# Kernel optimization log

Hardware: AMD Instinct MI355X
Metric: run time of the kernel (lower is better)

Reference implementation:

```python
import jax, jax.numpy as jnp
import numpy as np

B, T, C, L = 128, 512, 1024, 64
BLANK = C - 1          # keras ctc_batch_cost uses last class as blank
NEG = -1e9             # finite log-zero (grad-safe)
EPS = 1e-7             # keras.backend.epsilon()


def setup_inputs() -> dict:
    key = jax.random.key(0)
    k1, k2, k3, k4 = jax.random.split(key, 4)
    # y_pred: softmax probabilities, as ctc_batch_cost expects
    y_pred = jax.nn.softmax(jax.random.normal(k1, (B, T, C), dtype=jnp.float32), axis=-1)
    y_true = jax.random.randint(k2, (B, L), 0, BLANK).astype(jnp.int32)  # labels exclude blank
    input_length = jax.random.randint(k3, (B, 1), T // 2, T + 1).astype(jnp.int32)
    label_length = jax.random.randint(k4, (B, 1), L // 2, L + 1).astype(jnp.int32)
    return {"y_true": y_true, "y_pred": y_pred,
            "input_length": input_length, "label_length": label_length}


def _lse3(a, b, c):
    m = jnp.maximum(jnp.maximum(a, b), c)
    return m + jnp.log(jnp.exp(a - m) + jnp.exp(b - m) + jnp.exp(c - m))


def _ctc_loss(y_pred, y_true, input_length, label_length):
    # log probs, exactly as keras: log(y_pred + epsilon)
    logp = jnp.log(y_pred + EPS)                     # [B,T,C]
    Bsz, Tmax, _ = logp.shape
    Lm = y_true.shape[1]
    S = 2 * Lm + 1                                   # extended label length

    # extended labels: blank at even positions, labels at odd
    lab_ext = jnp.full((Bsz, S), BLANK, dtype=y_true.dtype).at[:, 1::2].set(y_true)
    s_idx = jnp.arange(S)
    in_len = input_length.reshape(-1)                # [B]
    lab_len = label_length.reshape(-1)               # [B]
    valid = s_idx[None, :] < (2 * lab_len[:, None] + 1)

    # skip transition s-2 -> s allowed iff lab[s] != blank and lab[s] != lab[s-2]
    lab_m2 = jnp.concatenate(
        [jnp.full((Bsz, 2), -1, dtype=lab_ext.dtype), lab_ext[:, :-2]], axis=1)
    skip_ok = (s_idx[None, :] >= 2) & (lab_ext != BLANK) & (lab_ext != lab_m2)

    # virtual alpha_{-1}: mass only at position 0
    alpha0 = jnp.broadcast_to(jnp.where(s_idx == 0, 0.0, NEG), (Bsz, S)).astype(logp.dtype)

    def step(alpha, inputs):
        lp_t, t = inputs                              # lp_t: [B,C]
        emit = jnp.take_along_axis(lp_t, lab_ext, axis=1)           # [B,S]
        s1 = jnp.concatenate([jnp.full((Bsz, 1), NEG, logp.dtype), alpha[:, :-1]], axis=1)
        s2 = jnp.concatenate([jnp.full((Bsz, 2), NEG, logp.dtype), alpha[:, :-2]], axis=1)
        s2 = jnp.where(skip_ok, s2, NEG)
        a = emit + _lse3(alpha, s1, s2)
        a = jnp.where(valid, a, NEG)
        # freeze alpha once t >= input_length (per-example variable T)
        a = jnp.where((t < in_len)[:, None], a, alpha)
        return a, None

    lp_tb = jnp.transpose(logp, (1, 0, 2))            # [T,B,C]
    alpha_T, _ = jax.lax.scan(step, alpha0, (lp_tb, jnp.arange(Tmax)))

    end_blank = 2 * lab_len                           # index of final blank
    end_label = 2 * lab_len - 1                       # index of final label
    a1 = jnp.take_along_axis(alpha_T, end_blank[:, None], axis=1)[:, 0]
    a2 = jnp.take_along_axis(alpha_T, end_label[:, None], axis=1)[:, 0]
    loss = -jnp.logaddexp(a1, a2)                     # [B]
    return loss[:, None]                              # keras returns [B,1]


def reference(y_true, y_pred, input_length, label_length):
    return _ctc_loss(y_pred, y_true, input_length, label_length)
```

## Files before the change

kernel.cpp:

```cpp
#include <hip/hip_runtime.h>


constexpr int Tmax   = 512;
constexpr int Cch    = 1024;
constexpr int Lm     = 64;
constexpr int BLANKC = Cch - 1;
constexpr int CH     = 64;
constexpr int NCH    = Tmax / CH;
constexpr int ROW    = 66;

#define NEGF (-1e9f)
#define EPSF (1e-7f)
#define LN2F (0.69314718055994530942f)

__device__ __forceinline__ float wave_shr1(float src, float fill) {
    int r = __builtin_amdgcn_update_dpp(__float_as_int(fill), __float_as_int(src),
                                        0x138, 0xf, 0xf, false);
    return __int_as_float(r);
}
__device__ __forceinline__ float lae2(float a, float b) {
    float m = fmaxf(a, b);
    return m + __builtin_log2f(__builtin_exp2f(a - m) + __builtin_exp2f(b - m));
}
__device__ __forceinline__ float lse3_2(float a, float b, float c) {
    float m = fmaxf(fmaxf(a, b), c);
    return m + __builtin_log2f(__builtin_exp2f(a - m) +
                               __builtin_exp2f(b - m) +
                               __builtin_exp2f(c - m));
}
__device__ __forceinline__ int clampi(int v, int lo, int hi) {
    return v < lo ? lo : (v > hi ? hi : v);
}

__global__ __launch_bounds__(1024, 1) void ctc_onekernel(
    const int*   __restrict__ y_true,
    const float* __restrict__ y_pred,
    const int*   __restrict__ in_len,
    const int*   __restrict__ lab_len,
    float*       __restrict__ out)
{
    const int b    = blockIdx.x;
    const int tid  = threadIdx.x;
    const int wave = tid >> 6;
    const int lane = tid & 63;

    __shared__ float Ebuf[2][CH * ROW];

    const int cls = y_true[b * Lm + lane];
    const int Tb  = clampi(in_len[b], 0, Tmax);
    const int lb  = clampi(lab_len[b], 0, Lm);
    const float* __restrict__ base = y_pred + (size_t)b * Tmax * Cch;

    auto gather = [&](int c) {
        const int tbase = c * CH;
        const int tt0   = wave - 1;
        float pc[5], pb[5];
#pragma unroll
        for (int k = 0; k < 5; ++k) {
            const int tt = tt0 + 15 * k;
            if (tt < CH) {
                const float* row = base + (size_t)(tbase + tt) * Cch;
                pc[k] = row[cls];
                pb[k] = row[BLANKC];
            }
        }
#pragma unroll
        for (int k = 0; k < 5; ++k) {
            const int tt = tt0 + 15 * k;
            if (tt < CH) {
                float* dst = &Ebuf[c & 1][tt * ROW];
                dst[lane] = __builtin_log2f(pc[k] + EPSF);
                if (lane == 0) dst[64] = __builtin_log2f(pb[k] + EPSF);
            }
        }
    };

    const int  cls_prev = __shfl_up(cls, 1, 64);
    const bool skip     = (lane >= 1) && (cls != cls_prev);
    const bool val_lo   = (lane <= lb);
    const bool val_hi   = (lane <  lb);
    const bool val_ex   = (lb == Lm);

    float a_lo = (lane == 0) ? 0.f : NEGF;
    float a_hi = NEGF;
    float a_ex = NEGF;

    if (wave != 0) gather(0);
    __syncthreads();

    for (int c = 0; c < NCH; ++c) {
        if (wave == 0) {
            const int tbase = c * CH;
            if (tbase < Tb) {
                const int steps = (Tb - tbase) < CH ? (Tb - tbase) : CH;
                const float* eb = Ebuf[c & 1];
                float rc[4], rb[4];
#pragma unroll
                for (int i = 0; i < 4; ++i) {
                    rc[i] = eb[i * ROW + lane];
                    rb[i] = eb[i * ROW + 64];
                }
                for (int i0 = 0; i0 < CH; i0 += 4) {
#pragma unroll
                    for (int j = 0; j < 4; ++j) {
                        const int i = i0 + j;
                        if (i >= steps) break;
                        const float e_c = rc[j];
                        const float e_b = rb[j];
                        const int tn = i + 4;
                        if (tn < CH) {
                            rc[j] = eb[tn * ROW + lane];
                            rb[j] = eb[tn * ROW + 64];
                        }
                        const float p_hi = wave_shr1(a_hi, NEGF);
                        float n_lo = e_b + lae2(a_lo, p_hi);
                        float n_hi = e_c + lse3_2(a_hi, a_lo, skip ? p_hi : NEGF);
                        float n_ex = e_b + lae2(a_ex, a_hi);
                        a_lo = val_lo ? n_lo : NEGF;
                        a_hi = val_hi ? n_hi : NEGF;
                        a_ex = val_ex ? n_ex : NEGF;
                    }
                    if (i0 + 4 >= steps) break;
                }
            }
        } else {
            if (c + 1 < NCH && (c + 1) * CH < Tb) gather(c + 1);
        }
        __syncthreads();
    }

    if (wave == 0) {
        const float a_end_blank = (lb == Lm) ? __shfl(a_ex, 63, 64)
                                             : __shfl(a_lo, lb, 64);
        const int   el_lane     = (lb >= 1) ? (lb - 1) : 0;
        const float a_end_label = (lb >= 1) ? __shfl(a_hi, el_lane, 64)
                                            : __shfl(a_lo, 0, 64);
        if (lane == 0) {
            out[b] = -LN2F * lae2(a_end_blank, a_end_label);
        }
    }
}

extern "C" void kernel_launch(void* const* d_in, const int* in_sizes, int n_in,
                              void* d_out, int out_size, void* d_ws, size_t ws_size,
                              hipStream_t stream) {
    const int*   y_true  = (const int*)  d_in[0];
    const float* y_pred  = (const float*)d_in[1];
    const int*   in_len  = (const int*)  d_in[2];
    const int*   lab_len = (const int*)  d_in[3];
    float*       out     = (float*)      d_out;

    ctc_onekernel<<<dim3(128), dim3(1024), 0, stream>>>(
        y_true, y_pred, in_len, lab_len, out);
}
```

Baseline: 416.5 us.

## Stage full probability rows into LDS via global_load_lds instead of scattered gathers

Gather waves now copy each full 4KB y_pred row into a per-wave LDS staging buffer using direct global-to-LDS loads, then read the label and blank probabilities from LDS. This replaces 64 scattered 4-byte loads per row with coalesced 16-byte loads. The block shrinks from 1024 to 512 threads (7 gather waves), and rows with t beyond the input length are skipped. The trade-off is reading the whole row (much more bytes) and waiting on each row serially with vmcnt(0), which can reduce memory-level parallelism.

```diff
diff --git a/kernel.cpp b/kernel.cpp
--- a/kernel.cpp
+++ b/kernel.cpp
@@ -8,6 +8,8 @@
 constexpr int CH     = 64;
 constexpr int NCH    = Tmax / CH;
 constexpr int ROW    = 66;
+constexpr int NB     = 128;
+constexpr int GW     = 7;
 
 #define NEGF (-1e9f)
 #define EPSF (1e-7f)
@@ -32,7 +34,7 @@
     return v < lo ? lo : (v > hi ? hi : v);
 }
 
-__global__ __launch_bounds__(1024, 1) void ctc_onekernel(
+__global__ __launch_bounds__(512, 1) void ctc_fused(
     const int*   __restrict__ y_true,
     const float* __restrict__ y_pred,
     const int*   __restrict__ in_len,
@@ -45,6 +47,7 @@
     const int lane = tid & 63;
 
     __shared__ float Ebuf[2][CH * ROW];
+    __shared__ float rowstage[GW][Cch];
 
     const int cls = y_true[b * Lm + lane];
     const int Tb  = clampi(in_len[b], 0, Tmax);
@@ -54,24 +57,28 @@
     auto gather = [&](int c) {
         const int tbase = c * CH;
         const int tt0   = wave - 1;
-        float pc[5], pb[5];
+        float* lbuf = rowstage[wave - 1];
+        for (int k = 0; k < 10; ++k) {
+            const int tt = tt0 + GW * k;
+            if (tt >= CH) break;
+            const int t = tbase + tt;
+            if (t >= Tb) continue;
+            const float* src = base + (size_t)t * Cch;
 #pragma unroll
-        for (int k = 0; k < 5; ++k) {
-            const int tt = tt0 + 15 * k;
-            if (tt < CH) {
-                const float* row = base + (size_t)(tbase + tt) * Cch;
-                pc[k] = row[cls];
-                pb[k] = row[BLANKC];
+            for (int j = 0; j < 4; ++j) {
+                __builtin_amdgcn_global_load_lds(
+                    (const __attribute__((address_space(1))) void*)
+                        (src + j * 256 + lane * 4),
+                    (__attribute__((address_space(3))) void*)(lbuf + j * 256),
+                    16, 0, 0);
             }
-        }
-#pragma unroll
-        for (int k = 0; k < 5; ++k) {
-            const int tt = tt0 + 15 * k;
-            if (tt < CH) {
-                float* dst = &Ebuf[c & 1][tt * ROW];
-                dst[lane] = __builtin_log2f(pc[k] + EPSF);
-                if (lane == 0) dst[64] = __builtin_log2f(pb[k] + EPSF);
-            }
+            asm volatile("s_waitcnt vmcnt(0)" ::: "memory");
+            const float pc = lbuf[cls];
+            const float pb = lbuf[BLANKC];
+            float* dst = &Ebuf[c & 1][tt * ROW];
+            dst[lane] = __builtin_log2f(pc + EPSF);
+            if (lane == 0) dst[64] = __builtin_log2f(pb + EPSF);
+            asm volatile("s_waitcnt lgkmcnt(0)" ::: "memory");
         }
     };
 
@@ -124,7 +131,8 @@
                 }
             }
         } else {
-            if (c + 1 < NCH && (c + 1) * CH < Tb) gather(c + 1);
+            const int n = c + 1;
+            if (n < NCH && n * CH < Tb) gather(n);
         }
         __syncthreads();
     }
@@ -150,6 +158,6 @@
     const int*   lab_len = (const int*)  d_in[3];
     float*       out     = (float*)      d_out;
 
-    ctc_onekernel<<<dim3(128), dim3(1024), 0, stream>>>(
+    ctc_fused<<<dim3(NB), dim3(512), 0, stream>>>(
         y_true, y_pred, in_len, lab_len, out);
 }
```

Measured after the change: 415.6 us. About the same (-0.2%).
